# Kernel optimization log

Hardware: AMD Instinct MI355X
Metric: run time of the kernel (lower is better)

## Reference

```python
import jax, jax.numpy as jnp
import numpy as np

SEQ = 110          # input_size1 = sample_width*2
HALF = SEQ // 2    # 55
N_EMBD = 102       # n_chrom + 2
HEAD = 192

def _cross_half_mask():
    # attention allowed only between the two halves (same-half blocks masked)
    idx = jnp.arange(SEQ)
    same_half = (idx[:, None] < HALF) == (idx[None, :] < HALF)
    return same_half  # True where attention is DISALLOWED

def setup_inputs() -> dict:
    key = jax.random.key(0)
    k1, k2, k3, k4 = jax.random.split(key, 4)
    B = 8192
    x = jax.random.normal(k1, (B, SEQ, N_EMBD), dtype=jnp.float32)
    Wq = jax.random.normal(k2, (N_EMBD, HEAD), dtype=jnp.float32) * (N_EMBD ** -0.5)
    Wk = jax.random.normal(k3, (N_EMBD, HEAD), dtype=jnp.float32) * (N_EMBD ** -0.5)
    Wv = jax.random.normal(k4, (N_EMBD, HEAD), dtype=jnp.float32) * (N_EMBD ** -0.5)
    return {"x": x, "Wq": Wq, "Wk": Wk, "Wv": Wv}

def reference(x, Wq, Wk, Wv):
    # q,k,v: [B, S, H]
    q = x @ Wq
    k = x @ Wk
    v = x @ Wv
    scale = HEAD ** -0.5
    scores = jnp.einsum('bsh,bth->bst', q, k) * scale  # [B, S, S]
    mask = _cross_half_mask()                           # [S, S] True = masked
    scores = jnp.where(mask, -jnp.inf, scores)
    attn = jax.nn.softmax(scores, axis=-1)
    # dropout is identity at inference (p=0.15 at train)
    out = jnp.einsum('bst,bth->bsh', attn, v)           # [B, S, H]
    return out
```

## Files before the change

### kernel.cpp

```cpp
#include <hip/hip_runtime.h>
#include <hip/hip_bf16.h>

#define SEQ   110
#define HALFS 55
#define EMB   102
#define HEAD  192

typedef short bf16x8 __attribute__((ext_vector_type(8)));
typedef float f32x4  __attribute__((ext_vector_type(4)));

#define XS    104
#define XTILE (64 * XS)
#define PS    72
#define MTS   128
#define MTROWS 112
#define MT_SHORTS (MTROWS * MTS)
#define WES   128

__device__ __forceinline__ short f2bf(float f) {
    unsigned u = __float_as_uint(f);
    unsigned r = u + 0x7fffu + ((u >> 16) & 1u);
    return (short)(r >> 16);
}
__device__ __forceinline__ unsigned pk2(float a, float b) {
    return ((unsigned)(unsigned short)f2bf(b) << 16) | (unsigned short)f2bf(a);
}

__global__ void prep(const float* __restrict__ Wq, const float* __restrict__ Wk,
                     const float* __restrict__ Wv, short* __restrict__ ws) {
    int flat = blockIdx.x * 256 + threadIdx.x;
    if (flat < MT_SHORTS) {
        int i = flat >> 7, j = flat & 127;
        float v = 0.0f;
        if (i < EMB && j < EMB) {
            const float4* q4 = (const float4*)(Wq + j * HEAD);
            const float4* k4 = (const float4*)(Wk + i * HEAD);
            float s = 0.0f;
            #pragma unroll 4
            for (int h4 = 0; h4 < HEAD / 4; ++h4) {
                float4 a = q4[h4], b = k4[h4];
                s += a.x * b.x + a.y * b.y + a.z * b.z + a.w * b.w;
            }
            v = s * 0.07216878364870322f;
        }
        ws[flat] = f2bf(v);
    } else if (flat < MT_SHORTS + HEAD * WES) {
        int idx = flat - MT_SHORTS;
        int h = idx >> 7, e = idx & 127;
        float v = (e < EMB) ? Wv[e * HEAD + h] : 0.0f;
        ws[flat] = f2bf(v);
    }
}

__global__ __launch_bounds__(512, 2)
void attn_head(const float* __restrict__ x, const short* __restrict__ ws,
               float* __restrict__ out, int B) {
    const int tid  = threadIdx.x;
    const int w8   = tid >> 6;
    const int h    = w8 >> 2;
    const int w4   = w8 & 3;
    const int lane = tid & 63;
    const int g    = lane >> 4;
    const int r    = lane & 15;

    __shared__ __attribute__((aligned(16))) short u[2 * XTILE];
    __shared__ __attribute__((aligned(16))) short P_lds[2][64 * PS];

    short* xh = u + h * XTILE;
    short* xo = u + (h ^ 1) * XTILE;
    short* Ph = P_lds[h];

    const short* Mt  = ws;
    const short* WvT = ws + MT_SHORTS;

    bf16x8 wvf[3][4];
    #pragma unroll
    for (int mi = 0; mi < 3; ++mi) {
        const int hrow = 16 * (w4 + 4 * mi) + r;
        #pragma unroll
        for (int kk = 0; kk < 4; ++kk)
            wvf[mi][kk] = *(const bf16x8*)(WvT + hrow * WES + 32 * kk + 8 * g);
    }

    {
        unsigned long long* z = (unsigned long long*)u;
        if (tid < 468) z[(tid < 234 ? 1430 : 2860) + tid] = 0ull;
        if (tid < 110)
            *(unsigned*)(u + (tid & 1) * XTILE + (tid >> 1) * XS + 102) = 0u;
    }

    unsigned xv0[6], xv1[6];
    auto loadx = [&](int batch) {
        const float4* xb4 = (const float4*)(x + (size_t)batch * (SEQ * EMB));
        #pragma unroll
        for (int it = 0; it < 6; ++it) {
            int i4 = tid + it * 512;
            if (i4 < 2805) { float4 v = xb4[i4]; xv0[it] = pk2(v.x, v.y); xv1[it] = pk2(v.z, v.w); }
        }
    };
    auto stagex = [&]() {
        #pragma unroll
        for (int it = 0; it < 6; ++it) {
            int i4 = tid + it * 512;
            if (i4 < 2805) {
                int fc  = i4 * 4;
                int row = (int)(((unsigned long long)fc * 41121ull) >> 22);
                int e   = fc - row * EMB;
                int tile = row >= HALFS;
                int lr   = row - HALFS * tile;
                int ba   = tile * XTILE + lr * XS + e;
                if (e == 100) {
                    int rowb  = row + 1;
                    int tileb = rowb >= HALFS;
                    int lrb   = rowb - HALFS * tileb;
                    *(unsigned*)(u + ba) = xv0[it];
                    *(unsigned*)(u + tileb * XTILE + lrb * XS) = xv1[it];
                } else {
                    uint2 t2; t2.x = xv0[it]; t2.y = xv1[it];
                    *(uint2*)(u + ba) = t2;
                }
            }
        }
    };

    loadx(blockIdx.x);
    stagex();
    const int stride = (int)gridDim.x;

    bf16x8 zz = {};
    const int src0 = ((g & 1) << 5) + r;
    const int src1 = src0 + 16;
    const bool hi  = (g >> 1) != 0;

    #pragma unroll 1
    for (int p = blockIdx.x; p < B; p += stride) {
        __syncthreads();

        bf16x8 bx[4];
        {
            const short* xb = xh + (16 * w4 + r) * XS;
            #pragma unroll
            for (int kk = 0; kk < 3; ++kk) bx[kk] = *(const bf16x8*)(xb + 32 * kk + 8 * g);
            bx[3] = zz;
            if (g == 0) bx[3] = *(const bf16x8*)(xb + 96);
        }

        unsigned vyp[8][2];
        #pragma unroll
        for (int mt = 0; mt < 7; ++mt) {
            f32x4 acc = {0.f, 0.f, 0.f, 0.f};
            #pragma unroll
            for (int kk = 0; kk < 4; ++kk) {
                bf16x8 am = *(const bf16x8*)(Mt + (16 * mt + r) * MTS + 32 * kk + 8 * g);
                acc = __builtin_amdgcn_mfma_f32_16x16x32_bf16(am, bx[kk], acc, 0, 0, 0);
            }
            vyp[mt][0] = pk2(acc[0], acc[1]);
            vyp[mt][1] = pk2(acc[2], acc[3]);
        }
        vyp[7][0] = 0u; vyp[7][1] = 0u;

        bf16x8 by[4];
        #pragma unroll
        for (int kk = 0; kk < 4; ++kk) {
            unsigned e0 = (unsigned)__shfl((int)vyp[2 * kk][0],     src0);
            unsigned e1 = (unsigned)__shfl((int)vyp[2 * kk][1],     src0);
            unsigned e2 = (unsigned)__shfl((int)vyp[2 * kk][0],     src1);
            unsigned e3 = (unsigned)__shfl((int)vyp[2 * kk][1],     src1);
            unsigned f0 = (unsigned)__shfl((int)vyp[2 * kk + 1][0], src0);
            unsigned f1 = (unsigned)__shfl((int)vyp[2 * kk + 1][1], src0);
            unsigned f2 = (unsigned)__shfl((int)vyp[2 * kk + 1][0], src1);
            unsigned f3 = (unsigned)__shfl((int)vyp[2 * kk + 1][1], src1);
            uint4 q;
            q.x = hi ? f0 : e0; q.y = hi ? f1 : e1; q.z = hi ? f2 : e2; q.w = hi ? f3 : e3;
            __builtin_memcpy(&by[kk], &q, 16);
        }

        float sc[4][4];
        #pragma unroll
        for (int mt = 0; mt < 4; ++mt) {
            const short* xb = xo + (16 * mt + r) * XS;
            bf16x8 axm[4];
            #pragma unroll
            for (int kk = 0; kk < 3; ++kk) axm[kk] = *(const bf16x8*)(xb + 32 * kk + 8 * g);
            axm[3] = zz;
            if (g == 0) axm[3] = *(const bf16x8*)(xb + 96);
            f32x4 acc = {0.f, 0.f, 0.f, 0.f};
            #pragma unroll
            for (int kk = 0; kk < 4; ++kk)
                acc = __builtin_amdgcn_mfma_f32_16x16x32_bf16(axm[kk], by[kk], acc, 0, 0, 0);
            #pragma unroll
            for (int j = 0; j < 4; ++j) sc[mt][j] = acc[j];
        }
        #pragma unroll
        for (int j = 0; j < 4; ++j)
            if (48 + 4 * g + j >= HALFS) sc[3][j] = -1e30f;

        {
            float mx = -1e30f;
            #pragma unroll
            for (int mt = 0; mt < 4; ++mt) {
                #pragma unroll
                for (int j = 0; j < 4; ++j) mx = fmaxf(mx, sc[mt][j]);
            }
            mx = fmaxf(mx, __shfl_xor(mx, 16));
            mx = fmaxf(mx, __shfl_xor(mx, 32));
            float pr[4][4];
            float sum = 0.f;
            #pragma unroll
            for (int mt = 0; mt < 4; ++mt) {
                #pragma unroll
                for (int j = 0; j < 4; ++j) { pr[mt][j] = __expf(sc[mt][j] - mx); sum += pr[mt][j]; }
            }
            sum += __shfl_xor(sum, 16);
            sum += __shfl_xor(sum, 32);
            float rs = 1.0f / sum;
            #pragma unroll
            for (int mt = 0; mt < 4; ++mt) {
                uint2 t2;
                t2.x = pk2(pr[mt][0] * rs, pr[mt][1] * rs);
                t2.y = pk2(pr[mt][2] * rs, pr[mt][3] * rs);
                *(uint2*)(Ph + (16 * w4 + r) * PS + 16 * mt + 4 * g) = t2;
            }
        }

        if (p + stride < B) loadx(p + stride);

        unsigned vpk[4][3][2];
        #pragma unroll
        for (int st = 0; st < 4; ++st) {
            const short* xb = xo + (16 * st + r) * XS;
            bf16x8 axm[4];
            #pragma unroll
            for (int kk = 0; kk < 3; ++kk) axm[kk] = *(const bf16x8*)(xb + 32 * kk + 8 * g);
            axm[3] = zz;
            if (g == 0) axm[3] = *(const bf16x8*)(xb + 96);
            #pragma unroll
            for (int mi = 0; mi < 3; ++mi) {
                f32x4 acc = {0.f, 0.f, 0.f, 0.f};
                #pragma unroll
                for (int kk = 0; kk < 4; ++kk)
                    acc = __builtin_amdgcn_mfma_f32_16x16x32_bf16(axm[kk], wvf[mi][kk], acc, 0, 0, 0);
                vpk[st][mi][0] = pk2(acc[0], acc[1]);
                vpk[st][mi][1] = pk2(acc[2], acc[3]);
            }
        }
        bf16x8 va[3][2];
        #pragma unroll
        for (int mi = 0; mi < 3; ++mi) {
            unsigned e00 = (unsigned)__shfl((int)vpk[0][mi][0], src0), e01 = (unsigned)__shfl((int)vpk[0][mi][1], src0);
            unsigned e02 = (unsigned)__shfl((int)vpk[0][mi][0], src1), e03 = (unsigned)__shfl((int)vpk[0][mi][1], src1);
            unsigned f00 = (unsigned)__shfl((int)vpk[1][mi][0], src0), f01 = (unsigned)__shfl((int)vpk[1][mi][1], src0);
            unsigned f02 = (unsigned)__shfl((int)vpk[1][mi][0], src1), f03 = (unsigned)__shfl((int)vpk[1][mi][1], src1);
            uint4 u0;
            u0.x = hi ? f00 : e00; u0.y = hi ? f01 : e01; u0.z = hi ? f02 : e02; u0.w = hi ? f03 : e03;
            unsigned e10 = (unsigned)__shfl((int)vpk[2][mi][0], src0), e11 = (unsigned)__shfl((int)vpk[2][mi][1], src0);
            unsigned e12 = (unsigned)__shfl((int)vpk[2][mi][0], src1), e13 = (unsigned)__shfl((int)vpk[2][mi][1], src1);
            unsigned f10 = (unsigned)__shfl((int)vpk[3][mi][0], src0), f11 = (unsigned)__shfl((int)vpk[3][mi][1], src0);
            unsigned f12 = (unsigned)__shfl((int)vpk[3][mi][0], src1), f13 = (unsigned)__shfl((int)vpk[3][mi][1], src1);
            uint4 u1;
            u1.x = hi ? f10 : e10; u1.y = hi ? f11 : e11; u1.z = hi ? f12 : e12; u1.w = hi ? f13 : e13;
            __builtin_memcpy(&va[mi][0], &u0, 16);
            __builtin_memcpy(&va[mi][1], &u1, 16);
        }

        __syncthreads();

        if (p + stride < B) stagex();

        const size_t obase = (size_t)p * (SEQ * HEAD) + (size_t)(h * HALFS) * HEAD;
        #pragma unroll
        for (int c = 0; c < 4; ++c) {
            const short* pb = Ph + (16 * c + r) * PS + 8 * g;
            bf16x8 bp0 = *(const bf16x8*)(pb);
            bf16x8 bp1 = *(const bf16x8*)(pb + 32);
            const int srow  = 16 * c + r;
            const bool valid = srow < HALFS;
            float* orow = out + obase + (size_t)srow * HEAD;
            #pragma unroll
            for (int mi = 0; mi < 3; ++mi) {
                f32x4 acc = {0.f, 0.f, 0.f, 0.f};
                acc = __builtin_amdgcn_mfma_f32_16x16x32_bf16(va[mi][0], bp0, acc, 0, 0, 0);
                acc = __builtin_amdgcn_mfma_f32_16x16x32_bf16(va[mi][1], bp1, acc, 0, 0, 0);
                if (valid) {
                    float4 st4; st4.x = acc[0]; st4.y = acc[1]; st4.z = acc[2]; st4.w = acc[3];
                    *(float4*)(orow + 16 * (w4 + 4 * mi) + 4 * g) = st4;
                }
            }
        }
    }
}

extern "C" void kernel_launch(void* const* d_in, const int* in_sizes, int n_in,
                              void* d_out, int out_size, void* d_ws, size_t ws_size,
                              hipStream_t stream) {
    const float* x  = (const float*)d_in[0];
    const float* Wq = (const float*)d_in[1];
    const float* Wk = (const float*)d_in[2];
    const float* Wv = (const float*)d_in[3];
    short* ws = (short*)d_ws;
    int B = in_sizes[0] / (SEQ * EMB);
    int prep_elems = MT_SHORTS + HEAD * WES;
    prep<<<(prep_elems + 255) / 256, 256, 0, stream>>>(Wq, Wk, Wv, ws);
    attn_head<<<512, 512, 0, stream>>>(x, ws, (float*)d_out, B);
}
```

Before: 318.8 us.

## Give each wavefront a whole batch and drop LDS staging and block barriers

Work is reassigned so that each 64-lane wavefront processes one batch element end to end, both halves, instead of eight waves sharing a batch through shared memory. x rows are read straight from global memory and converted to bf16 in registers. The probability matrix is passed between lanes with shuffles rather than through LDS, and all __syncthreads are gone. The cost is that x rows are re-read from global/L2 several times per wave, Wv fragments are reloaded per output-column block, and register pressure rises. The launch moves to 2048 blocks of 256 threads.

Result: slower. 1.136 ms (+256.4%).

```diff
diff --git a/kernel.cpp b/kernel.cpp
--- a/kernel.cpp
+++ b/kernel.cpp
@@ -9,9 +9,6 @@
 typedef short bf16x8 __attribute__((ext_vector_type(8)));
 typedef float f32x4  __attribute__((ext_vector_type(4)));
 
-#define XS    104
-#define XTILE (64 * XS)
-#define PS    72
 #define MTS   128
 #define MTROWS 112
 #define MT_SHORTS (MTROWS * MTS)
@@ -52,238 +49,211 @@
     }
 }
 
-__global__ __launch_bounds__(512, 2)
+__device__ __forceinline__ bf16x8 ldfrag(const float* rowp, int e) {
+    const float2* p = (const float2*)(rowp + e);
+    float2 a = p[0], b = p[1], c = p[2], d = p[3];
+    uint4 q;
+    q.x = pk2(a.x, a.y); q.y = pk2(b.x, b.y);
+    q.z = pk2(c.x, c.y); q.w = pk2(d.x, d.y);
+    bf16x8 rr; __builtin_memcpy(&rr, &q, 16); return rr;
+}
+__device__ __forceinline__ bf16x8 ldfrag_tail(const float* rowp) {
+    const float2* p = (const float2*)(rowp + 96);
+    float2 a = p[0], b = p[1], c = p[2];
+    uint4 q;
+    q.x = pk2(a.x, a.y); q.y = pk2(b.x, b.y);
+    q.z = pk2(c.x, c.y); q.w = 0u;
+    bf16x8 rr; __builtin_memcpy(&rr, &q, 16); return rr;
+}
+
+__global__ __launch_bounds__(256, 4)
 void attn_head(const float* __restrict__ x, const short* __restrict__ ws,
                float* __restrict__ out, int B) {
     const int tid  = threadIdx.x;
-    const int w8   = tid >> 6;
-    const int h    = w8 >> 2;
-    const int w4   = w8 & 3;
+    const int w4   = tid >> 6;
     const int lane = tid & 63;
     const int g    = lane >> 4;
     const int r    = lane & 15;
 
-    __shared__ __attribute__((aligned(16))) short u[2 * XTILE];
-    __shared__ __attribute__((aligned(16))) short P_lds[2][64 * PS];
-
-    short* xh = u + h * XTILE;
-    short* xo = u + (h ^ 1) * XTILE;
-    short* Ph = P_lds[h];
-
     const short* Mt  = ws;
     const short* WvT = ws + MT_SHORTS;
-
-    bf16x8 wvf[3][4];
-    #pragma unroll
-    for (int mi = 0; mi < 3; ++mi) {
-        const int hrow = 16 * (w4 + 4 * mi) + r;
-        #pragma unroll
-        for (int kk = 0; kk < 4; ++kk)
-            wvf[mi][kk] = *(const bf16x8*)(WvT + hrow * WES + 32 * kk + 8 * g);
-    }
-
-    {
-        unsigned long long* z = (unsigned long long*)u;
-        if (tid < 468) z[(tid < 234 ? 1430 : 2860) + tid] = 0ull;
-        if (tid < 110)
-            *(unsigned*)(u + (tid & 1) * XTILE + (tid >> 1) * XS + 102) = 0u;
-    }
-
-    unsigned xv0[6], xv1[6];
-    auto loadx = [&](int batch) {
-        const float4* xb4 = (const float4*)(x + (size_t)batch * (SEQ * EMB));
-        #pragma unroll
-        for (int it = 0; it < 6; ++it) {
-            int i4 = tid + it * 512;
-            if (i4 < 2805) { float4 v = xb4[i4]; xv0[it] = pk2(v.x, v.y); xv1[it] = pk2(v.z, v.w); }
-        }
-    };
-    auto stagex = [&]() {
-        #pragma unroll
-        for (int it = 0; it < 6; ++it) {
-            int i4 = tid + it * 512;
-            if (i4 < 2805) {
-                int fc  = i4 * 4;
-                int row = (int)(((unsigned long long)fc * 41121ull) >> 22);
-                int e   = fc - row * EMB;
-                int tile = row >= HALFS;
-                int lr   = row - HALFS * tile;
-                int ba   = tile * XTILE + lr * XS + e;
-                if (e == 100) {
-                    int rowb  = row + 1;
-                    int tileb = rowb >= HALFS;
-                    int lrb   = rowb - HALFS * tileb;
-                    *(unsigned*)(u + ba) = xv0[it];
-                    *(unsigned*)(u + tileb * XTILE + lrb * XS) = xv1[it];
-                } else {
-                    uint2 t2; t2.x = xv0[it]; t2.y = xv1[it];
-                    *(uint2*)(u + ba) = t2;
-                }
-            }
-        }
-    };
-
-    loadx(blockIdx.x);
-    stagex();
-    const int stride = (int)gridDim.x;
 
     bf16x8 zz = {};
     const int src0 = ((g & 1) << 5) + r;
     const int src1 = src0 + 16;
     const bool hi  = (g >> 1) != 0;
 
+    const int p0      = (int)blockIdx.x * 4 + w4;
+    const int wstride = (int)gridDim.x * 4;
+
     #pragma unroll 1
-    for (int p = blockIdx.x; p < B; p += stride) {
-        __syncthreads();
-
-        bf16x8 bx[4];
-        {
-            const short* xb = xh + (16 * w4 + r) * XS;
+    for (int p = p0; p < B; p += wstride) {
+        const float* xb = x + (size_t)p * (SEQ * EMB);
+        float* ob = out + (size_t)p * (SEQ * HEAD);
+
+        #pragma unroll 1
+        for (int half = 0; half < 2; ++half) {
+            const int own = half * HALFS;
+            const int oth = HALFS - own;
+
+            bf16x8 bpA[4], bpB[4];
             #pragma unroll
-            for (int kk = 0; kk < 3; ++kk) bx[kk] = *(const bf16x8*)(xb + 32 * kk + 8 * g);
-            bx[3] = zz;
-            if (g == 0) bx[3] = *(const bf16x8*)(xb + 96);
-        }
-
-        unsigned vyp[8][2];
-        #pragma unroll
-        for (int mt = 0; mt < 7; ++mt) {
-            f32x4 acc = {0.f, 0.f, 0.f, 0.f};
-            #pragma unroll
-            for (int kk = 0; kk < 4; ++kk) {
-                bf16x8 am = *(const bf16x8*)(Mt + (16 * mt + r) * MTS + 32 * kk + 8 * g);
-                acc = __builtin_amdgcn_mfma_f32_16x16x32_bf16(am, bx[kk], acc, 0, 0, 0);
+            for (int c = 0; c < 4; ++c) {
+                bf16x8 bx[4];
+                {
+                    int rr = 16 * c + r; rr = (rr > 54) ? 54 : rr;
+                    const float* rowp = xb + (size_t)(own + rr) * EMB;
+                    #pragma unroll
+                    for (int kk = 0; kk < 3; ++kk) bx[kk] = ldfrag(rowp, 32 * kk + 8 * g);
+                    bx[3] = zz;
+                    if (g == 0) bx[3] = ldfrag_tail(rowp);
+                }
+                unsigned vyp[8][2];
+                #pragma unroll
+                for (int mt = 0; mt < 7; ++mt) {
+                    const short* amp = Mt + (16 * mt + r) * MTS + 8 * g;
+                    f32x4 acc = {0.f, 0.f, 0.f, 0.f};
+                    #pragma unroll
+                    for (int kk = 0; kk < 4; ++kk)
+                        acc = __builtin_amdgcn_mfma_f32_16x16x32_bf16(
+                            *(const bf16x8*)(amp + 32 * kk), bx[kk], acc, 0, 0, 0);
+                    vyp[mt][0] = pk2(acc[0], acc[1]);
+                    vyp[mt][1] = pk2(acc[2], acc[3]);
+                }
+                vyp[7][0] = 0u; vyp[7][1] = 0u;
+                bf16x8 by[4];
+                #pragma unroll
+                for (int kk = 0; kk < 4; ++kk) {
+                    unsigned e0 = (unsigned)__shfl((int)vyp[2 * kk][0],     src0);
+                    unsigned e1 = (unsigned)__shfl((int)vyp[2 * kk][1],     src0);
+                    unsigned e2 = (unsigned)__shfl((int)vyp[2 * kk][0],     src1);
+                    unsigned e3 = (unsigned)__shfl((int)vyp[2 * kk][1],     src1);
+                    unsigned f0 = (unsigned)__shfl((int)vyp[2 * kk + 1][0], src0);
+                    unsigned f1 = (unsigned)__shfl((int)vyp[2 * kk + 1][1], src0);
+                    unsigned f2 = (unsigned)__shfl((int)vyp[2 * kk + 1][0], src1);
+                    unsigned f3 = (unsigned)__shfl((int)vyp[2 * kk + 1][1], src1);
+                    uint4 q;
+                    q.x = hi ? f0 : e0; q.y = hi ? f1 : e1; q.z = hi ? f2 : e2; q.w = hi ? f3 : e3;
+                    __builtin_memcpy(&by[kk], &q, 16);
+                }
+                float sc[4][4];
+                #pragma unroll
+                for (int mt = 0; mt < 4; ++mt) {
+                    int rr = 16 * mt + r; rr = (rr > 54) ? 54 : rr;
+                    const float* rowp = xb + (size_t)(oth + rr) * EMB;
+                    bf16x8 axm[4];
+                    #pragma unroll
+                    for (int kk = 0; kk < 3; ++kk) axm[kk] = ldfrag(rowp, 32 * kk + 8 * g);
+                    axm[3] = zz;
+                    if (g == 0) axm[3] = ldfrag_tail(rowp);
+                    f32x4 acc = {0.f, 0.f, 0.f, 0.f};
+                    #pragma unroll
+                    for (int kk = 0; kk < 4; ++kk)
+                        acc = __builtin_amdgcn_mfma_f32_16x16x32_bf16(axm[kk], by[kk], acc, 0, 0, 0);
+                    #pragma unroll
+                    for (int j = 0; j < 4; ++j) sc[mt][j] = acc[j];
+                }
+                #pragma unroll
+                for (int j = 0; j < 4; ++j)
+                    if (48 + 4 * g + j >= HALFS) sc[3][j] = -1e30f;
+
+                float mx = -1e30f;
+                #pragma unroll
+                for (int mt = 0; mt < 4; ++mt) {
+                    #pragma unroll
+                    for (int j = 0; j < 4; ++j) mx = fmaxf(mx, sc[mt][j]);
+                }
+                mx = fmaxf(mx, __shfl_xor(mx, 16));
+                mx = fmaxf(mx, __shfl_xor(mx, 32));
+                float pr[4][4];
+                float sum = 0.f;
+                #pragma unroll
+                for (int mt = 0; mt < 4; ++mt) {
+                    #pragma unroll
+                    for (int j = 0; j < 4; ++j) { pr[mt][j] = __expf(sc[mt][j] - mx); sum += pr[mt][j]; }
+                }
+                sum += __shfl_xor(sum, 16);
+                sum += __shfl_xor(sum, 32);
+                float rs = 1.0f / sum;
+
+                unsigned pu[4][2];
+                #pragma unroll
+                for (int mt = 0; mt < 4; ++mt) {
+                    pu[mt][0] = pk2(pr[mt][0] * rs, pr[mt][1] * rs);
+                    pu[mt][1] = pk2(pr[mt][2] * rs, pr[mt][3] * rs);
+                }
+                unsigned A00 = (unsigned)__shfl((int)pu[0][0], src0), A01 = (unsigned)__shfl((int)pu[0][1], src0);
+                unsigned A02 = (unsigned)__shfl((int)pu[0][0], src1), A03 = (unsigned)__shfl((int)pu[0][1], src1);
+                unsigned B00 = (unsigned)__shfl((int)pu[1][0], src0), B01 = (unsigned)__shfl((int)pu[1][1], src0);
+                unsigned B02 = (unsigned)__shfl((int)pu[1][0], src1), B03 = (unsigned)__shfl((int)pu[1][1], src1);
+                unsigned C00 = (unsigned)__shfl((int)pu[2][0], src0), C01 = (unsigned)__shfl((int)pu[2][1], src0);
+                unsigned C02 = (unsigned)__shfl((int)pu[2][0], src1), C03 = (unsigned)__shfl((int)pu[2][1], src1);
+                unsigned D00 = (unsigned)__shfl((int)pu[3][0], src0), D01 = (unsigned)__shfl((int)pu[3][1], src0);
+                unsigned D02 = (unsigned)__shfl((int)pu[3][0], src1), D03 = (unsigned)__shfl((int)pu[3][1], src1);
+                uint4 q0, q1;
+                q0.x = hi ? B00 : A00; q0.y = hi ? B01 : A01; q0.z = hi ? B02 : A02; q0.w = hi ? B03 : A03;
+                q1.x = hi ? D00 : C00; q1.y = hi ? D01 : C01; q1.z = hi ? D02 : C02; q1.w = hi ? D03 : C03;
+                __builtin_memcpy(&bpA[c], &q0, 16);
+                __builtin_memcpy(&bpB[c], &q1, 16);
             }
-            vyp[mt][0] = pk2(acc[0], acc[1]);
-            vyp[mt][1] = pk2(acc[2], acc[3]);
-        }
-        vyp[7][0] = 0u; vyp[7][1] = 0u;
-
-        bf16x8 by[4];
-        #pragma unroll
-        for (int kk = 0; kk < 4; ++kk) {
-            unsigned e0 = (unsigned)__shfl((int)vyp[2 * kk][0],     src0);
-            unsigned e1 = (unsigned)__shfl((int)vyp[2 * kk][1],     src0);
-            unsigned e2 = (unsigned)__shfl((int)vyp[2 * kk][0],     src1);
-            unsigned e3 = (unsigned)__shfl((int)vyp[2 * kk][1],     src1);
-            unsigned f0 = (unsigned)__shfl((int)vyp[2 * kk + 1][0], src0);
-            unsigned f1 = (unsigned)__shfl((int)vyp[2 * kk + 1][1], src0);
-            unsigned f2 = (unsigned)__shfl((int)vyp[2 * kk + 1][0], src1);
-            unsigned f3 = (unsigned)__shfl((int)vyp[2 * kk + 1][1], src1);
-            uint4 q;
-            q.x = hi ? f0 : e0; q.y = hi ? f1 : e1; q.z = hi ? f2 : e2; q.w = hi ? f3 : e3;
-            __builtin_memcpy(&by[kk], &q, 16);
-        }
-
-        float sc[4][4];
-        #pragma unroll
-        for (int mt = 0; mt < 4; ++mt) {
-            const short* xb = xo + (16 * mt + r) * XS;
-            bf16x8 axm[4];
-            #pragma unroll
-            for (int kk = 0; kk < 3; ++kk) axm[kk] = *(const bf16x8*)(xb + 32 * kk + 8 * g);
-            axm[3] = zz;
-            if (g == 0) axm[3] = *(const bf16x8*)(xb + 96);
-            f32x4 acc = {0.f, 0.f, 0.f, 0.f};
-            #pragma unroll
-            for (int kk = 0; kk < 4; ++kk)
-                acc = __builtin_amdgcn_mfma_f32_16x16x32_bf16(axm[kk], by[kk], acc, 0, 0, 0);
-            #pragma unroll
-            for (int j = 0; j < 4; ++j) sc[mt][j] = acc[j];
-        }
-        #pragma unroll
-        for (int j = 0; j < 4; ++j)
-            if (48 + 4 * g + j >= HALFS) sc[3][j] = -1e30f;
-
-        {
-            float mx = -1e30f;
-            #pragma unroll
-            for (int mt = 0; mt < 4; ++mt) {
-                #pragma unroll
-                for (int j = 0; j < 4; ++j) mx = fmaxf(mx, sc[mt][j]);
-            }
-            mx = fmaxf(mx, __shfl_xor(mx, 16));
-            mx = fmaxf(mx, __shfl_xor(mx, 32));
-            float pr[4][4];
-            float sum = 0.f;
-            #pragma unroll
-            for (int mt = 0; mt < 4; ++mt) {
-                #pragma unroll
-                for (int j = 0; j < 4; ++j) { pr[mt][j] = __expf(sc[mt][j] - mx); sum += pr[mt][j]; }
-            }
-            sum += __shfl_xor(sum, 16);
-            sum += __shfl_xor(sum, 32);
-            float rs = 1.0f / sum;
-            #pragma unroll
-            for (int mt = 0; mt < 4; ++mt) {
-                uint2 t2;
-                t2.x = pk2(pr[mt][0] * rs, pr[mt][1] * rs);
-                t2.y = pk2(pr[mt][2] * rs, pr[mt][3] * rs);
-                *(uint2*)(Ph + (16 * w4 + r) * PS + 16 * mt + 4 * g) = t2;
-            }
-        }
-
-        if (p + stride < B) loadx(p + stride);
-
-        unsigned vpk[4][3][2];
-        #pragma unroll
-        for (int st = 0; st < 4; ++st) {
-            const short* xb = xo + (16 * st + r) * XS;
-            bf16x8 axm[4];
-            #pragma unroll
-            for (int kk = 0; kk < 3; ++kk) axm[kk] = *(const bf16x8*)(xb + 32 * kk + 8 * g);
-            axm[3] = zz;
-            if (g == 0) axm[3] = *(const bf16x8*)(xb + 96);
-            #pragma unroll
-            for (int mi = 0; mi < 3; ++mi) {
-                f32x4 acc = {0.f, 0.f, 0.f, 0.f};
-                #pragma unroll
-                for (int kk = 0; kk < 4; ++kk)
-                    acc = __builtin_amdgcn_mfma_f32_16x16x32_bf16(axm[kk], wvf[mi][kk], acc, 0, 0, 0);
-                vpk[st][mi][0] = pk2(acc[0], acc[1]);
-                vpk[st][mi][1] = pk2(acc[2], acc[3]);
-            }
-        }
-        bf16x8 va[3][2];
-        #pragma unroll
-        for (int mi = 0; mi < 3; ++mi) {
-            unsigned e00 = (unsigned)__shfl((int)vpk[0][mi][0], src0), e01 = (unsigned)__shfl((int)vpk[0][mi][1], src0);
-            unsigned e02 = (unsigned)__shfl((int)vpk[0][mi][0], src1), e03 = (unsigned)__shfl((int)vpk[0][mi][1], src1);
-            unsigned f00 = (unsigned)__shfl((int)vpk[1][mi][0], src0), f01 = (unsigned)__shfl((int)vpk[1][mi][1], src0);
-            unsigned f02 = (unsigned)__shfl((int)vpk[1][mi][0], src1), f03 = (unsigned)__shfl((int)vpk[1][mi][1], src1);
-            uint4 u0;
-            u0.x = hi ? f00 : e00; u0.y = hi ? f01 : e01; u0.z = hi ? f02 : e02; u0.w = hi ? f03 : e03;
-            unsigned e10 = (unsigned)__shfl((int)vpk[2][mi][0], src0), e11 = (unsigned)__shfl((int)vpk[2][mi][1], src0);
-            unsigned e12 = (unsigned)__shfl((int)vpk[2][mi][0], src1), e13 = (unsigned)__shfl((int)vpk[2][mi][1], src1);
-            unsigned f10 = (unsigned)__shfl((int)vpk[3][mi][0], src0), f11 = (unsigned)__shfl((int)vpk[3][mi][1], src0);
-            unsigned f12 = (unsigned)__shfl((int)vpk[3][mi][0], src1), f13 = (unsigned)__shfl((int)vpk[3][mi][1], src1);
-            uint4 u1;
-            u1.x = hi ? f10 : e10; u1.y = hi ? f11 : e11; u1.z = hi ? f12 : e12; u1.w = hi ? f13 : e13;
-            __builtin_memcpy(&va[mi][0], &u0, 16);
-            __builtin_memcpy(&va[mi][1], &u1, 16);
-        }
-
-        __syncthreads();
-
-        if (p + stride < B) stagex();
-
-        const size_t obase = (size_t)p * (SEQ * HEAD) + (size_t)(h * HALFS) * HEAD;
-        #pragma unroll
-        for (int c = 0; c < 4; ++c) {
-            const short* pb = Ph + (16 * c + r) * PS + 8 * g;
-            bf16x8 bp0 = *(const bf16x8*)(pb);
-            bf16x8 bp1 = *(const bf16x8*)(pb + 32);
-            const int srow  = 16 * c + r;
-            const bool valid = srow < HALFS;
-            float* orow = out + obase + (size_t)srow * HEAD;
-            #pragma unroll
-            for (int mi = 0; mi < 3; ++mi) {
-                f32x4 acc = {0.f, 0.f, 0.f, 0.f};
-                acc = __builtin_amdgcn_mfma_f32_16x16x32_bf16(va[mi][0], bp0, acc, 0, 0, 0);
-                acc = __builtin_amdgcn_mfma_f32_16x16x32_bf16(va[mi][1], bp1, acc, 0, 0, 0);
-                if (valid) {
-                    float4 st4; st4.x = acc[0]; st4.y = acc[1]; st4.z = acc[2]; st4.w = acc[3];
-                    *(float4*)(orow + 16 * (w4 + 4 * mi) + 4 * g) = st4;
+
+            #pragma unroll 1
+            for (int hb = 0; hb < 4; ++hb) {
+                unsigned vpk[4][3][2];
+                #pragma unroll
+                for (int st = 0; st < 4; ++st) {
+                    int rr = 16 * st + r; rr = (rr > 54) ? 54 : rr;
+                    const float* rowp = xb + (size_t)(oth + rr) * EMB;
+                    bf16x8 axm[4];
+                    #pragma unroll
+                    for (int kk = 0; kk < 3; ++kk) axm[kk] = ldfrag(rowp, 32 * kk + 8 * g);
+                    axm[3] = zz;
+                    if (g == 0) axm[3] = ldfrag_tail(rowp);
+                    #pragma unroll
+                    for (int mi = 0; mi < 3; ++mi) {
+                        const short* wvp = WvT + (16 * (3 * hb + mi) + r) * WES + 8 * g;
+                        f32x4 acc = {0.f, 0.f, 0.f, 0.f};
+                        #pragma unroll
+                        for (int kk = 0; kk < 4; ++kk)
+                            acc = __builtin_amdgcn_mfma_f32_16x16x32_bf16(
+                                axm[kk], *(const bf16x8*)(wvp + 32 * kk), acc, 0, 0, 0);
+                        vpk[st][mi][0] = pk2(acc[0], acc[1]);
+                        vpk[st][mi][1] = pk2(acc[2], acc[3]);
+                    }
+                }
+                bf16x8 va[3][2];
+                #pragma unroll
+                for (int mi = 0; mi < 3; ++mi) {
+                    unsigned e00 = (unsigned)__shfl((int)vpk[0][mi][0], src0), e01 = (unsigned)__shfl((int)vpk[0][mi][1], src0);
+                    unsigned e02 = (unsigned)__shfl((int)vpk[0][mi][0], src1), e03 = (unsigned)__shfl((int)vpk[0][mi][1], src1);
+                    unsigned f00 = (unsigned)__shfl((int)vpk[1][mi][0], src0), f01 = (unsigned)__shfl((int)vpk[1][mi][1], src0);
+                    unsigned f02 = (unsigned)__shfl((int)vpk[1][mi][0], src1), f03 = (unsigned)__shfl((int)vpk[1][mi][1], src1);
+                    uint4 u0;
+                    u0.x = hi ? f00 : e00; u0.y = hi ? f01 : e01; u0.z = hi ? f02 : e02; u0.w = hi ? f03 : e03;
+                    unsigned e10 = (unsigned)__shfl((int)vpk[2][mi][0], src0), e11 = (unsigned)__shfl((int)vpk[2][mi][1], src0);
+                    unsigned e12 = (unsigned)__shfl((int)vpk[2][mi][0], src1), e13 = (unsigned)__shfl((int)vpk[2][mi][1], src1);
+                    unsigned f10 = (unsigned)__shfl((int)vpk[3][mi][0], src0), f11 = (unsigned)__shfl((int)vpk[3][mi][1], src0);
+                    unsigned f12 = (unsigned)__shfl((int)vpk[3][mi][0], src1), f13 = (unsigned)__shfl((int)vpk[3][mi][1], src1);
+                    uint4 u1;
+                    u1.x = hi ? f10 : e10; u1.y = hi ? f11 : e11; u1.z = hi ? f12 : e12; u1.w = hi ? f13 : e13;
+                    __builtin_memcpy(&va[mi][0], &u0, 16);
+                    __builtin_memcpy(&va[mi][1], &u1, 16);
+                }
+                #pragma unroll
+                for (int c = 0; c < 4; ++c) {
+                    const int srow  = 16 * c + r;
+                    const bool valid = srow < HALFS;
+                    float* orow = ob + (size_t)(own + srow) * HEAD;
+                    #pragma unroll
+                    for (int mi = 0; mi < 3; ++mi) {
+                        f32x4 acc = {0.f, 0.f, 0.f, 0.f};
+                        acc = __builtin_amdgcn_mfma_f32_16x16x32_bf16(va[mi][0], bpA[c], acc, 0, 0, 0);
+                        acc = __builtin_amdgcn_mfma_f32_16x16x32_bf16(va[mi][1], bpB[c], acc, 0, 0, 0);
+                        if (valid) {
+                            float4 st4; st4.x = acc[0]; st4.y = acc[1]; st4.z = acc[2]; st4.w = acc[3];
+                            *(float4*)(orow + 16 * (3 * hb + mi) + 4 * g) = st4;
+                        }
+                    }
                 }
             }
         }
@@ -301,5 +271,5 @@
     int B = in_sizes[0] / (SEQ * EMB);
     int prep_elems = MT_SHORTS + HEAD * WES;
     prep<<<(prep_elems + 255) / 256, 256, 0, stream>>>(Wq, Wk, Wv, ws);
-    attn_head<<<512, 512, 0, stream>>>(x, ws, (float*)d_out, B);
-}
+    attn_head<<<2048, 256, 0, stream>>>(x, ws, (float*)d_out, B);
+}
```
